# Kernel tuning notes

Hardware: AMD Instinct MI355X
Metric: run time of the kernel (lower is better)

## Reference

```python
import jax, jax.numpy as jnp
import numpy as np

BLOCK = 16
N1, N2, RANK = 64, 64, 64
# E2M1 (NVFP4) representable magnitudes
_FP4_GRID = jnp.array([0.0, 0.5, 1.0, 1.5, 2.0, 3.0, 4.0, 6.0], dtype=jnp.float32)
_FP4_MIDS = (_FP4_GRID[1:] + _FP4_GRID[:-1]) / 2.0


def quantize_to_nvfp4(x, block_size=BLOCK):
    """Per-block (last dim, block_size=16) NVFP4 fake-quant: amax scale to 6.0, round to E2M1 grid, dequant."""
    shape = x.shape
    xb = x.reshape(shape[:-1] + (shape[-1] // block_size, block_size))
    amax = jnp.max(jnp.abs(xb), axis=-1, keepdims=True)
    scale = jnp.maximum(amax / 6.0, 1e-8)
    y = xb / scale
    idx = jnp.searchsorted(_FP4_MIDS, jnp.abs(y), side='right')  # nearest grid index
    q = _FP4_GRID[idx] * jnp.sign(y)
    return (q * scale).reshape(shape)


def setup_inputs() -> dict:
    key = jax.random.key(0)
    ks = jax.random.split(key, 6)
    B, S, n, m, r = 4, 2048, 4096, 4096, RANK
    return {
        'x': jax.random.normal(ks[0], (B, S, n), dtype=jnp.float32),
        'smooth_scale': jax.random.uniform(ks[1], (n,), dtype=jnp.float32, minval=0.2, maxval=2.0),
        'a_q': jax.random.normal(ks[2], (m, r), dtype=jnp.float32) * 0.05,
        'b_q': jax.random.normal(ks[3], (N1, r), dtype=jnp.float32) * 0.1,
        'c_q_t': jax.random.normal(ks[4], (r, N2), dtype=jnp.float32) * 0.1,
        'bias': jax.random.normal(ks[5], (m,), dtype=jnp.float32),
    }


def reference(x, smooth_scale, a_q, b_q, c_q_t, bias):
    # smooth + activation quant
    x_q = quantize_to_nvfp4(x * smooth_scale, BLOCK)
    # reshape (..., n) -> (..., n1, n2)
    x_3d = x_q.reshape(x.shape[:-1] + (N1, N2))
    # contract C: F.linear(x_3d, c_q_t) -> (..., n1, r)
    h1 = jnp.einsum('bsij,rj->bsir', x_3d, c_q_t)
    # contract B: (h1 * B).sum over n1 -> (..., r)
    h2 = jnp.einsum('bsir,ir->bsr', h1, b_q)
    # contract A: h2 @ A.T + bias -> (..., m)
    out = jnp.einsum('bsr,mr->bsm', h2, a_q) + bias
    return out
```

## Files before the change

### kernel.cpp

```cpp
#include <hip/hip_runtime.h>

typedef float f32x4 __attribute__((ext_vector_type(4)));
typedef short s16x8 __attribute__((ext_vector_type(8)));
typedef short s16x4 __attribute__((ext_vector_type(4)));
typedef unsigned short u16;

#define N_COLS 4096
#define RANK 64

__device__ __forceinline__ unsigned f_asuint(float f) { union { float f; unsigned u; } v; v.f = f; return v.u; }
__device__ __forceinline__ float f_asfloat(unsigned u) { union { unsigned u; float f; } v; v.u = u; return v.f; }
__device__ __forceinline__ short f2bf(float f) {
  unsigned u = f_asuint(f);
  return (short)((u + 0x7fffu + ((u >> 16) & 1u)) >> 16);
}

__global__ __launch_bounds__(256) void k_prep(const float* __restrict__ b_q,
                                              const float* __restrict__ c_q_t,
                                              const float* __restrict__ a_q,
                                              u16* __restrict__ W,
                                              u16* __restrict__ a_bf) {
  int idx = blockIdx.x * 256 + threadIdx.x;
  if (idx < RANK * N_COLS) {
    int r = idx >> 12;
    int n = idx & 4095;
    W[idx] = (u16)f2bf(b_q[(n >> 6) * RANK + r] * c_q_t[(r << 6) + (n & 63)]);
  } else {
    int j = idx - RANK * N_COLS;
    a_bf[j] = (u16)f2bf(a_q[j]);
  }
}

__global__ __launch_bounds__(512, 4) void k_qgemm1(const float* __restrict__ x,
                                                   const float* __restrict__ smooth,
                                                   const u16* __restrict__ W,
                                                   u16* __restrict__ h2b) {
  const int t0 = blockIdx.x * 16;
  const int wave = threadIdx.x >> 6;
  const int lane = threadIdx.x & 63;
  const int quad = lane >> 4;
  const int tl = lane & 15;
  const int K0 = wave * 512 + quad * 8;

  const float* xp = x + (size_t)(t0 + tl) * N_COLS + K0;
  const float* sp = smooth + K0;
  const u16* wp0 = W + (size_t)tl * N_COLS + K0;
  const u16* wp1 = wp0 + 16 * N_COLS;
  const u16* wp2 = wp0 + 32 * N_COLS;
  const u16* wp3 = wp0 + 48 * N_COLS;

  f32x4 acc0 = {0.f, 0.f, 0.f, 0.f};
  f32x4 acc1 = {0.f, 0.f, 0.f, 0.f};
  f32x4 acc2 = {0.f, 0.f, 0.f, 0.f};
  f32x4 acc3 = {0.f, 0.f, 0.f, 0.f};

  for (int s = 0; s < 16; ++s) {
    const int o = s * 32;
    f32x4 xa = __builtin_nontemporal_load(reinterpret_cast<const f32x4*>(xp + o));
    f32x4 xb = __builtin_nontemporal_load(reinterpret_cast<const f32x4*>(xp + o + 4));
    f32x4 sa = *reinterpret_cast<const f32x4*>(sp + o);
    f32x4 sb = *reinterpret_cast<const f32x4*>(sp + o + 4);
    float xs[8];
    xs[0] = xa.x * sa.x; xs[1] = xa.y * sa.y; xs[2] = xa.z * sa.z; xs[3] = xa.w * sa.w;
    xs[4] = xb.x * sb.x; xs[5] = xb.y * sb.y; xs[6] = xb.z * sb.z; xs[7] = xb.w * sb.w;

    float amax = fabsf(xs[0]);
#pragma unroll
    for (int j = 1; j < 8; ++j) amax = fmaxf(amax, fabsf(xs[j]));
    amax = fmaxf(amax, __shfl_xor(amax, 16));
    float scale = fmaxf(amax * (1.0f / 6.0f), 1e-8f);

    const float th0 = 0.25f * scale, th1 = 0.75f * scale, th2 = 1.25f * scale,
                th3 = 1.75f * scale, th4 = 2.5f * scale, th5 = 3.5f * scale,
                th6 = 5.0f * scale;
    s16x8 af;
#pragma unroll
    for (int j = 0; j < 8; ++j) {
      float ax = fabsf(xs[j]);
      float q = (ax >= th0) ? 0.5f : 0.0f;
      q = (ax >= th1) ? 1.0f : q;
      q = (ax >= th2) ? 1.5f : q;
      q = (ax >= th3) ? 2.0f : q;
      q = (ax >= th4) ? 3.0f : q;
      q = (ax >= th5) ? 4.0f : q;
      q = (ax >= th6) ? 6.0f : q;
      float xq = q * scale;
      xq = f_asfloat(f_asuint(xq) | (f_asuint(xs[j]) & 0x80000000u));
      af[j] = f2bf(xq);
    }

    s16x8 b0 = *reinterpret_cast<const s16x8*>(wp0 + o);
    s16x8 b1 = *reinterpret_cast<const s16x8*>(wp1 + o);
    s16x8 b2 = *reinterpret_cast<const s16x8*>(wp2 + o);
    s16x8 b3 = *reinterpret_cast<const s16x8*>(wp3 + o);

    acc0 = __builtin_amdgcn_mfma_f32_16x16x32_bf16(af, b0, acc0, 0, 0, 0);
    acc1 = __builtin_amdgcn_mfma_f32_16x16x32_bf16(af, b1, acc1, 0, 0, 0);
    acc2 = __builtin_amdgcn_mfma_f32_16x16x32_bf16(af, b2, acc2, 0, 0, 0);
    acc3 = __builtin_amdgcn_mfma_f32_16x16x32_bf16(af, b3, acc3, 0, 0, 0);
  }

  __shared__ float red[8 * 16 * 64];
  float* rw = red + wave * 1024 + (quad * 4) * 64 + tl;
#pragma unroll
  for (int reg = 0; reg < 4; ++reg) {
    rw[reg * 64 + 0]  = acc0[reg];
    rw[reg * 64 + 16] = acc1[reg];
    rw[reg * 64 + 32] = acc2[reg];
    rw[reg * 64 + 48] = acc3[reg];
  }
  __syncthreads();
  if (threadIdx.x < 256) {
    const f32x4* r4 = reinterpret_cast<const f32x4*>(red);
    f32x4 v = r4[threadIdx.x];
#pragma unroll
    for (int p = 1; p < 8; ++p) {
      f32x4 u = r4[p * 256 + threadIdx.x];
      v.x += u.x; v.y += u.y; v.z += u.z; v.w += u.w;
    }
    int t = threadIdx.x >> 4;
    int rr = (threadIdx.x & 15) * 4;
    s16x4 o4;
    o4.x = f2bf(v.x); o4.y = f2bf(v.y); o4.z = f2bf(v.z); o4.w = f2bf(v.w);
    *reinterpret_cast<s16x4*>(h2b + (size_t)(t0 + t) * RANK + rr) = o4;
  }
}

__global__ __launch_bounds__(256, 4) void k_gemm2(const u16* __restrict__ h2b,
                                                  const u16* __restrict__ a_bf,
                                                  const float* __restrict__ bias,
                                                  float* __restrict__ out) {
  const int t0 = blockIdx.y * 32;
  const int m0 = blockIdx.x * 256;
  const int wave = threadIdx.x >> 6;
  const int lane = threadIdx.x & 63;
  const int quad = lane >> 4;
  const int tl = lane & 15;

  const u16* hp0 = h2b + (size_t)(t0 + tl) * RANK + quad * 8;
  const u16* hp1 = hp0 + 16 * RANK;
  const u16* ap = a_bf + (size_t)(m0 + wave * 64 + tl) * RANK + quad * 8;

  f32x4 acc[2][4] = {};

#pragma unroll
  for (int o = 0; o < 64; o += 32) {
    s16x8 a0 = *reinterpret_cast<const s16x8*>(hp0 + o);
    s16x8 a1 = *reinterpret_cast<const s16x8*>(hp1 + o);
#pragma unroll
    for (int mg = 0; mg < 4; ++mg) {
      s16x8 bfr = *reinterpret_cast<const s16x8*>(ap + (size_t)mg * 16 * RANK + o);
      acc[0][mg] = __builtin_amdgcn_mfma_f32_16x16x32_bf16(a0, bfr, acc[0][mg], 0, 0, 0);
      acc[1][mg] = __builtin_amdgcn_mfma_f32_16x16x32_bf16(a1, bfr, acc[1][mg], 0, 0, 0);
    }
  }

  __shared__ float tile[16 * 260];
#pragma unroll
  for (int tg = 0; tg < 2; ++tg) {
    if (tg) __syncthreads();
#pragma unroll
    for (int mg = 0; mg < 4; ++mg)
#pragma unroll
      for (int reg = 0; reg < 4; ++reg)
        tile[(quad * 4 + reg) * 260 + wave * 64 + mg * 16 + tl] = acc[tg][mg][reg];
    __syncthreads();
#pragma unroll
    for (int i = 0; i < 4; ++i) {
      int idx = threadIdx.x + i * 256;
      int row = idx >> 6;
      int c4 = (idx & 63) << 2;
      f32x4 v = *reinterpret_cast<const f32x4*>(tile + row * 260 + c4);
      f32x4 b = *reinterpret_cast<const f32x4*>(bias + m0 + c4);
      f32x4 ov;
      ov.x = v.x + b.x; ov.y = v.y + b.y; ov.z = v.z + b.z; ov.w = v.w + b.w;
      __builtin_nontemporal_store(ov,
        reinterpret_cast<f32x4*>(out + (size_t)(t0 + tg * 16 + row) * N_COLS + m0 + c4));
    }
  }
}

extern "C" void kernel_launch(void* const* d_in, const int* in_sizes, int n_in,
                              void* d_out, int out_size, void* d_ws, size_t ws_size,
                              hipStream_t stream) {
  const float* x      = (const float*)d_in[0];
  const float* smooth = (const float*)d_in[1];
  const float* a_q    = (const float*)d_in[2];
  const float* b_q    = (const float*)d_in[3];
  const float* c_q_t  = (const float*)d_in[4];
  const float* bias   = (const float*)d_in[5];
  float* out = (float*)d_out;

  const int T = in_sizes[0] / N_COLS;

  u16* W    = (u16*)d_ws;
  u16* a_bf = (u16*)((char*)d_ws + 524288);
  u16* h2b  = (u16*)((char*)d_ws + 1048576);

  k_prep<<<2048, 256, 0, stream>>>(b_q, c_q_t, a_q, W, a_bf);
  k_qgemm1<<<T / 16, 512, 0, stream>>>(x, smooth, W, h2b);
  dim3 g2(N_COLS / 256, T / 32);
  k_gemm2<<<g2, 256, 0, stream>>>(h2b, a_bf, bias, out);
}
```

Baseline: 276.2 us.

## Fuse quantized first GEMM and rank-to-output GEMM into a single kernel

Merges the two GEMM kernels into one, so the rank-64 intermediate h2 for each 16-token tile stays in shared memory instead of going through global memory as bf16. Each wave then multiplies that tile against its 512-column slice of A and writes output plus bias directly. This removes a kernel launch and the h2 round trip, and it lets input reads and output writes from different blocks overlap. The cost is extra block-wide barriers inside the output loop, even though each wave only touches its own tile, and more shared memory per block, which can lower occupancy.

```diff
diff --git a/kernel.cpp b/kernel.cpp
--- a/kernel.cpp
+++ b/kernel.cpp
@@ -2,11 +2,11 @@
 
 typedef float f32x4 __attribute__((ext_vector_type(4)));
 typedef short s16x8 __attribute__((ext_vector_type(8)));
-typedef short s16x4 __attribute__((ext_vector_type(4)));
 typedef unsigned short u16;
 
 #define N_COLS 4096
 #define RANK 64
+#define H2S 68
 
 __device__ __forceinline__ unsigned f_asuint(float f) { union { float f; unsigned u; } v; v.f = f; return v.u; }
 __device__ __forceinline__ float f_asfloat(unsigned u) { union { unsigned u; float f; } v; v.u = u; return v.f; }
@@ -31,87 +31,93 @@
   }
 }
 
-__global__ __launch_bounds__(512, 4) void k_qgemm1(const float* __restrict__ x,
-                                                   const float* __restrict__ smooth,
-                                                   const u16* __restrict__ W,
-                                                   u16* __restrict__ h2b) {
+__global__ __launch_bounds__(512, 4) void k_fused(const float* __restrict__ x,
+                                                  const float* __restrict__ smooth,
+                                                  const u16* __restrict__ W,
+                                                  const u16* __restrict__ a_bf,
+                                                  const float* __restrict__ bias,
+                                                  float* __restrict__ out) {
+  __shared__ float smem[8 * 16 * H2S];
+  __shared__ float h2f[16 * H2S];
+
   const int t0 = blockIdx.x * 16;
   const int wave = threadIdx.x >> 6;
   const int lane = threadIdx.x & 63;
   const int quad = lane >> 4;
   const int tl = lane & 15;
-  const int K0 = wave * 512 + quad * 8;
 
-  const float* xp = x + (size_t)(t0 + tl) * N_COLS + K0;
-  const float* sp = smooth + K0;
-  const u16* wp0 = W + (size_t)tl * N_COLS + K0;
-  const u16* wp1 = wp0 + 16 * N_COLS;
-  const u16* wp2 = wp0 + 32 * N_COLS;
-  const u16* wp3 = wp0 + 48 * N_COLS;
+  {
+    const int K0 = wave * 512 + quad * 8;
+    const float* xp = x + (size_t)(t0 + tl) * N_COLS + K0;
+    const float* sp = smooth + K0;
+    const u16* wp0 = W + (size_t)tl * N_COLS + K0;
+    const u16* wp1 = wp0 + 16 * N_COLS;
+    const u16* wp2 = wp0 + 32 * N_COLS;
+    const u16* wp3 = wp0 + 48 * N_COLS;
 
-  f32x4 acc0 = {0.f, 0.f, 0.f, 0.f};
-  f32x4 acc1 = {0.f, 0.f, 0.f, 0.f};
-  f32x4 acc2 = {0.f, 0.f, 0.f, 0.f};
-  f32x4 acc3 = {0.f, 0.f, 0.f, 0.f};
+    f32x4 acc0 = {0.f, 0.f, 0.f, 0.f};
+    f32x4 acc1 = {0.f, 0.f, 0.f, 0.f};
+    f32x4 acc2 = {0.f, 0.f, 0.f, 0.f};
+    f32x4 acc3 = {0.f, 0.f, 0.f, 0.f};
 
-  for (int s = 0; s < 16; ++s) {
-    const int o = s * 32;
-    f32x4 xa = __builtin_nontemporal_load(reinterpret_cast<const f32x4*>(xp + o));
-    f32x4 xb = __builtin_nontemporal_load(reinterpret_cast<const f32x4*>(xp + o + 4));
-    f32x4 sa = *reinterpret_cast<const f32x4*>(sp + o);
-    f32x4 sb = *reinterpret_cast<const f32x4*>(sp + o + 4);
-    float xs[8];
-    xs[0] = xa.x * sa.x; xs[1] = xa.y * sa.y; xs[2] = xa.z * sa.z; xs[3] = xa.w * sa.w;
-    xs[4] = xb.x * sb.x; xs[5] = xb.y * sb.y; xs[6] = xb.z * sb.z; xs[7] = xb.w * sb.w;
+    for (int s = 0; s < 16; ++s) {
+      const int o = s * 32;
+      f32x4 xa = __builtin_nontemporal_load(reinterpret_cast<const f32x4*>(xp + o));
+      f32x4 xb = __builtin_nontemporal_load(reinterpret_cast<const f32x4*>(xp + o + 4));
+      f32x4 sa = *reinterpret_cast<const f32x4*>(sp + o);
+      f32x4 sb = *reinterpret_cast<const f32x4*>(sp + o + 4);
+      float xs[8];
+      xs[0] = xa.x * sa.x; xs[1] = xa.y * sa.y; xs[2] = xa.z * sa.z; xs[3] = xa.w * sa.w;
+      xs[4] = xb.x * sb.x; xs[5] = xb.y * sb.y; xs[6] = xb.z * sb.z; xs[7] = xb.w * sb.w;
 
-    float amax = fabsf(xs[0]);
+      float amax = fabsf(xs[0]);
 #pragma unroll
-    for (int j = 1; j < 8; ++j) amax = fmaxf(amax, fabsf(xs[j]));
-    amax = fmaxf(amax, __shfl_xor(amax, 16));
-    float scale = fmaxf(amax * (1.0f / 6.0f), 1e-8f);
+      for (int j = 1; j < 8; ++j) amax = fmaxf(amax, fabsf(xs[j]));
+      amax = fmaxf(amax, __shfl_xor(amax, 16));
+      float scale = fmaxf(amax * (1.0f / 6.0f), 1e-8f);
 
-    const float th0 = 0.25f * scale, th1 = 0.75f * scale, th2 = 1.25f * scale,
-                th3 = 1.75f * scale, th4 = 2.5f * scale, th5 = 3.5f * scale,
-                th6 = 5.0f * scale;
-    s16x8 af;
+      const float th0 = 0.25f * scale, th1 = 0.75f * scale, th2 = 1.25f * scale,
+                  th3 = 1.75f * scale, th4 = 2.5f * scale, th5 = 3.5f * scale,
+                  th6 = 5.0f * scale;
+      s16x8 af;
 #pragma unroll
-    for (int j = 0; j < 8; ++j) {
-      float ax = fabsf(xs[j]);
-      float q = (ax >= th0) ? 0.5f : 0.0f;
-      q = (ax >= th1) ? 1.0f : q;
-      q = (ax >= th2) ? 1.5f : q;
-      q = (ax >= th3) ? 2.0f : q;
-      q = (ax >= th4) ? 3.0f : q;
-      q = (ax >= th5) ? 4.0f : q;
-      q = (ax >= th6) ? 6.0f : q;
-      float xq = q * scale;
-      xq = f_asfloat(f_asuint(xq) | (f_asuint(xs[j]) & 0x80000000u));
-      af[j] = f2bf(xq);
+      for (int j = 0; j < 8; ++j) {
+        float ax = fabsf(xs[j]);
+        float q = (ax >= th0) ? 0.5f : 0.0f;
+        q = (ax >= th1) ? 1.0f : q;
+        q = (ax >= th2) ? 1.5f : q;
+        q = (ax >= th3) ? 2.0f : q;
+        q = (ax >= th4) ? 3.0f : q;
+        q = (ax >= th5) ? 4.0f : q;
+        q = (ax >= th6) ? 6.0f : q;
+        float xq = q * scale;
+        xq = f_asfloat(f_asuint(xq) | (f_asuint(xs[j]) & 0x80000000u));
+        af[j] = f2bf(xq);
+      }
+
+      s16x8 b0 = *reinterpret_cast<const s16x8*>(wp0 + o);
+      s16x8 b1 = *reinterpret_cast<const s16x8*>(wp1 + o);
+      s16x8 b2 = *reinterpret_cast<const s16x8*>(wp2 + o);
+      s16x8 b3 = *reinterpret_cast<const s16x8*>(wp3 + o);
+
+      acc0 = __builtin_amdgcn_mfma_f32_16x16x32_bf16(af, b0, acc0, 0, 0, 0);
+      acc1 = __builtin_amdgcn_mfma_f32_16x16x32_bf16(af, b1, acc1, 0, 0, 0);
+      acc2 = __builtin_amdgcn_mfma_f32_16x16x32_bf16(af, b2, acc2, 0, 0, 0);
+      acc3 = __builtin_amdgcn_mfma_f32_16x16x32_bf16(af, b3, acc3, 0, 0, 0);
     }
 
-    s16x8 b0 = *reinterpret_cast<const s16x8*>(wp0 + o);
-    s16x8 b1 = *reinterpret_cast<const s16x8*>(wp1 + o);
-    s16x8 b2 = *reinterpret_cast<const s16x8*>(wp2 + o);
-    s16x8 b3 = *reinterpret_cast<const s16x8*>(wp3 + o);
-
-    acc0 = __builtin_amdgcn_mfma_f32_16x16x32_bf16(af, b0, acc0, 0, 0, 0);
-    acc1 = __builtin_amdgcn_mfma_f32_16x16x32_bf16(af, b1, acc1, 0, 0, 0);
-    acc2 = __builtin_amdgcn_mfma_f32_16x16x32_bf16(af, b2, acc2, 0, 0, 0);
-    acc3 = __builtin_amdgcn_mfma_f32_16x16x32_bf16(af, b3, acc3, 0, 0, 0);
-  }
-
-  __shared__ float red[8 * 16 * 64];
-  float* rw = red + wave * 1024 + (quad * 4) * 64 + tl;
+    float* rw = smem + wave * 1024 + (quad * 4) * 64 + tl;
 #pragma unroll
-  for (int reg = 0; reg < 4; ++reg) {
-    rw[reg * 64 + 0]  = acc0[reg];
-    rw[reg * 64 + 16] = acc1[reg];
-    rw[reg * 64 + 32] = acc2[reg];
-    rw[reg * 64 + 48] = acc3[reg];
+    for (int reg = 0; reg < 4; ++reg) {
+      rw[reg * 64 + 0]  = acc0[reg];
+      rw[reg * 64 + 16] = acc1[reg];
+      rw[reg * 64 + 32] = acc2[reg];
+      rw[reg * 64 + 48] = acc3[reg];
+    }
   }
   __syncthreads();
   if (threadIdx.x < 256) {
-    const f32x4* r4 = reinterpret_cast<const f32x4*>(red);
+    const f32x4* r4 = reinterpret_cast<const f32x4*>(smem);
     f32x4 v = r4[threadIdx.x];
 #pragma unroll
     for (int p = 1; p < 8; ++p) {
@@ -120,62 +126,51 @@
     }
     int t = threadIdx.x >> 4;
     int rr = (threadIdx.x & 15) * 4;
-    s16x4 o4;
-    o4.x = f2bf(v.x); o4.y = f2bf(v.y); o4.z = f2bf(v.z); o4.w = f2bf(v.w);
-    *reinterpret_cast<s16x4*>(h2b + (size_t)(t0 + t) * RANK + rr) = o4;
+    *reinterpret_cast<f32x4*>(h2f + t * H2S + rr) = v;
   }
-}
+  __syncthreads();
 
-__global__ __launch_bounds__(256, 4) void k_gemm2(const u16* __restrict__ h2b,
-                                                  const u16* __restrict__ a_bf,
-                                                  const float* __restrict__ bias,
-                                                  float* __restrict__ out) {
-  const int t0 = blockIdx.y * 32;
-  const int m0 = blockIdx.x * 256;
-  const int wave = threadIdx.x >> 6;
-  const int lane = threadIdx.x & 63;
-  const int quad = lane >> 4;
-  const int tl = lane & 15;
+  f32x4 a0 = *reinterpret_cast<const f32x4*>(h2f + tl * H2S + quad * 8);
+  f32x4 a1 = *reinterpret_cast<const f32x4*>(h2f + tl * H2S + quad * 8 + 4);
+  f32x4 a2 = *reinterpret_cast<const f32x4*>(h2f + tl * H2S + 32 + quad * 8);
+  f32x4 a3 = *reinterpret_cast<const f32x4*>(h2f + tl * H2S + 32 + quad * 8 + 4);
+  s16x8 af_lo, af_hi;
+  af_lo[0] = f2bf(a0.x); af_lo[1] = f2bf(a0.y); af_lo[2] = f2bf(a0.z); af_lo[3] = f2bf(a0.w);
+  af_lo[4] = f2bf(a1.x); af_lo[5] = f2bf(a1.y); af_lo[6] = f2bf(a1.z); af_lo[7] = f2bf(a1.w);
+  af_hi[0] = f2bf(a2.x); af_hi[1] = f2bf(a2.y); af_hi[2] = f2bf(a2.z); af_hi[3] = f2bf(a2.w);
+  af_hi[4] = f2bf(a3.x); af_hi[5] = f2bf(a3.y); af_hi[6] = f2bf(a3.z); af_hi[7] = f2bf(a3.w);
 
-  const u16* hp0 = h2b + (size_t)(t0 + tl) * RANK + quad * 8;
-  const u16* hp1 = hp0 + 16 * RANK;
-  const u16* ap = a_bf + (size_t)(m0 + wave * 64 + tl) * RANK + quad * 8;
+  float* wtile = smem + wave * (16 * H2S);
 
-  f32x4 acc[2][4] = {};
-
+  for (int mg = 0; mg < 8; ++mg) {
+    const int m_base = wave * 512 + mg * 64;
+    f32x4 acc[4] = {};
 #pragma unroll
-  for (int o = 0; o < 64; o += 32) {
-    s16x8 a0 = *reinterpret_cast<const s16x8*>(hp0 + o);
-    s16x8 a1 = *reinterpret_cast<const s16x8*>(hp1 + o);
+    for (int sub = 0; sub < 4; ++sub) {
+      const u16* ap = a_bf + (size_t)(m_base + sub * 16 + tl) * RANK + quad * 8;
+      s16x8 blo = *reinterpret_cast<const s16x8*>(ap);
+      s16x8 bhi = *reinterpret_cast<const s16x8*>(ap + 32);
+      acc[sub] = __builtin_amdgcn_mfma_f32_16x16x32_bf16(af_lo, blo, acc[sub], 0, 0, 0);
+      acc[sub] = __builtin_amdgcn_mfma_f32_16x16x32_bf16(af_hi, bhi, acc[sub], 0, 0, 0);
+    }
+    __syncthreads();
 #pragma unroll
-    for (int mg = 0; mg < 4; ++mg) {
-      s16x8 bfr = *reinterpret_cast<const s16x8*>(ap + (size_t)mg * 16 * RANK + o);
-      acc[0][mg] = __builtin_amdgcn_mfma_f32_16x16x32_bf16(a0, bfr, acc[0][mg], 0, 0, 0);
-      acc[1][mg] = __builtin_amdgcn_mfma_f32_16x16x32_bf16(a1, bfr, acc[1][mg], 0, 0, 0);
-    }
-  }
-
-  __shared__ float tile[16 * 260];
-#pragma unroll
-  for (int tg = 0; tg < 2; ++tg) {
-    if (tg) __syncthreads();
-#pragma unroll
-    for (int mg = 0; mg < 4; ++mg)
+    for (int sub = 0; sub < 4; ++sub)
 #pragma unroll
       for (int reg = 0; reg < 4; ++reg)
-        tile[(quad * 4 + reg) * 260 + wave * 64 + mg * 16 + tl] = acc[tg][mg][reg];
+        wtile[(quad * 4 + reg) * H2S + sub * 16 + tl] = acc[sub][reg];
     __syncthreads();
 #pragma unroll
     for (int i = 0; i < 4; ++i) {
-      int idx = threadIdx.x + i * 256;
-      int row = idx >> 6;
-      int c4 = (idx & 63) << 2;
-      f32x4 v = *reinterpret_cast<const f32x4*>(tile + row * 260 + c4);
-      f32x4 b = *reinterpret_cast<const f32x4*>(bias + m0 + c4);
+      int idx = lane + i * 64;
+      int row = idx >> 4;
+      int c4 = (idx & 15) << 2;
+      f32x4 v = *reinterpret_cast<const f32x4*>(wtile + row * H2S + c4);
+      f32x4 b = *reinterpret_cast<const f32x4*>(bias + m_base + c4);
       f32x4 ov;
       ov.x = v.x + b.x; ov.y = v.y + b.y; ov.z = v.z + b.z; ov.w = v.w + b.w;
       __builtin_nontemporal_store(ov,
-        reinterpret_cast<f32x4*>(out + (size_t)(t0 + tg * 16 + row) * N_COLS + m0 + c4));
+        reinterpret_cast<f32x4*>(out + (size_t)(t0 + row) * N_COLS + m_base + c4));
     }
   }
 }
@@ -195,10 +190,7 @@
 
   u16* W    = (u16*)d_ws;
   u16* a_bf = (u16*)((char*)d_ws + 524288);
-  u16* h2b  = (u16*)((char*)d_ws + 1048576);
 
   k_prep<<<2048, 256, 0, stream>>>(b_q, c_q_t, a_q, W, a_bf);
-  k_qgemm1<<<T / 16, 512, 0, stream>>>(x, smooth, W, h2b);
-  dim3 g2(N_COLS / 256, T / 32);
-  k_gemm2<<<g2, 256, 0, stream>>>(h2b, a_bf, bias, out);
+  k_fused<<<T / 16, 512, 0, stream>>>(x, smooth, W, a_bf, bias, out);
 }
```

Measured after the change: 288.1 us. +4.3%, slower.
